# Optimization experiments

Measured on AMD Instinct MI355X. Metric: run time of the kernel, lower is better.

## Reference

```python
import jax, jax.numpy as jnp
import numpy as np

IN_FEATURES = 512
OUT_FEATURES = 10
NEURONS_STRUCTURES = [64, 128, 256, 512]
REPETITIONS = 5
NUM_ACTIVATIONS = 4  # relu, tanh, sigmoid, gelu (exact erf, matching torch nn.GELU)
NUM_MODELS = NUM_ACTIVATIONS * REPETITIONS * len(NEURONS_STRUCTURES)  # 80
TOTAL_HIDDEN = sum(NEURONS_STRUCTURES) * REPETITIONS * NUM_ACTIVATIONS  # 19200
BATCH = 1024


def _build_neuron_model_id():
    # Mirrors ParallelMLPs.__init__ construction order:
    # for act -> for rep -> for structure: assign consecutive model ids
    ids = []
    m = 0
    for _act in range(NUM_ACTIVATIONS):
        for _rep in range(REPETITIONS):
            for n in NEURONS_STRUCTURES:
                ids += [m] * n
                m += 1
    return np.asarray(ids, dtype=np.int32)


def setup_inputs() -> dict:
    key = jax.random.key(0)
    k1, k2, k3, k4, k5 = jax.random.split(key, 5)
    x = jax.random.normal(k1, (BATCH, IN_FEATURES), dtype=jnp.float32)
    hidden_w = jax.random.normal(k2, (TOTAL_HIDDEN, IN_FEATURES), dtype=jnp.float32) * 0.05
    hidden_b = jax.random.normal(k3, (TOTAL_HIDDEN,), dtype=jnp.float32) * 0.05
    out_w = jax.random.normal(k4, (OUT_FEATURES, TOTAL_HIDDEN), dtype=jnp.float32) * 0.05
    out_b = jax.random.normal(k5, (NUM_MODELS, OUT_FEATURES), dtype=jnp.float32) * 0.05
    neuron_model_id = jnp.asarray(_build_neuron_model_id())
    return {"x": x, "hidden_w": hidden_w, "hidden_b": hidden_b,
            "out_w": out_w, "out_b": out_b, "neuron_model_id": neuron_model_id}


def reference(x, hidden_w, hidden_b, out_w, out_b, neuron_model_id):
    # Shared hidden linear: [B, H]
    h = x @ hidden_w.T + hidden_b
    # Per-block activations on equal contiguous chunks of the hidden dim
    split = TOTAL_HIDDEN // NUM_ACTIVATIONS
    acts = [jax.nn.relu, jnp.tanh, jax.nn.sigmoid,
            lambda t: jax.nn.gelu(t, approximate=False)]
    a = jnp.concatenate(
        [f(h[:, i * split:(i + 1) * split]) for i, f in enumerate(acts)], axis=1)
    # Ragged grouped out-projection: contrib[h, b, o] = a[b, h] * out_w[o, h]
    contrib = a.T[:, :, None] * out_w.T[:, None, :]  # [H, B, O]
    grouped = jax.ops.segment_sum(contrib, neuron_model_id,
                                  num_segments=NUM_MODELS)  # [M, B, O]
    return jnp.transpose(grouped, (1, 0, 2)) + out_b[None, :, :]  # [B, M, O]
```

## Files before the change

### kernel.cpp

```cpp
#include <hip/hip_runtime.h>
#include <hip/hip_bf16.h>
#include <cstdint>
#include <cstddef>


typedef unsigned short u16;
typedef unsigned int u32;
typedef __bf16 bf16x8 __attribute__((ext_vector_type(8)));
typedef float f32x4 __attribute__((ext_vector_type(4)));

__device__ __forceinline__ u16 f2bf(float f) {
  u32 u = __builtin_bit_cast(u32, f);
  u += 0x7fffu + ((u >> 16) & 1u);
  return (u16)(u >> 16);
}

__device__ __forceinline__ void async16(void* l, const void* g) {
  __builtin_amdgcn_global_load_lds(
      (__attribute__((address_space(1))) void*)(void*)g,
      (__attribute__((address_space(3))) void*)l, 16, 0, 0);
}

__device__ __forceinline__ void drain_vm() {
  asm volatile("s_waitcnt vmcnt(0)" ::: "memory");
}

__global__ __launch_bounds__(256) void cvt_kernel(
    const float4* __restrict__ xs, uint2* __restrict__ xd, int nx4,
    const float4* __restrict__ ws, uint2* __restrict__ wd, int nw4) {
  int i = blockIdx.x * blockDim.x + threadIdx.x;
  if (i >= nx4 + nw4) return;
  const float4* s; uint2* d; int j;
  if (i < nx4) { s = xs; d = xd; j = i; }
  else         { s = ws; d = wd; j = i - nx4; }
  float4 f = s[j];
  uint2 o;
  o.x = (u32)f2bf(f.x) | ((u32)f2bf(f.y) << 16);
  o.y = (u32)f2bf(f.z) | ((u32)f2bf(f.w) << 16);
  d[j] = o;
}

__global__ __launch_bounds__(256, 2) void gemm_act_kernel(
    const u16* __restrict__ A,
    const u16* __restrict__ Bw,
    const float* __restrict__ hbias,
    u16* __restrict__ aout) {
  __shared__ char lds[65536];
  const int t = threadIdx.x;
  const int lane = t & 63;
  const int w = t >> 6;
  const int c = blockIdx.x & 7;
  const int L = c * 150 + (blockIdx.x >> 3);
  const int bx = L >> 3;
  const int by = L & 7;
  const int row0 = by * 128;
  const int col0 = bx * 128;
  const int wr = w >> 1, wc = w & 1;

  f32x4 acc[4][4];
#pragma unroll
  for (int m = 0; m < 4; ++m)
#pragma unroll
    for (int n = 0; n < 4; ++n)
#pragma unroll
      for (int r = 0; r < 4; ++r) acc[m][n][r] = 0.f;

  const int srow = t >> 3;
  const int sc8 = t & 7;

  auto stage = [&](int buf, int kt) {
    const int k0 = kt * 64 + sc8 * 8;
#pragma unroll
    for (int i = 0; i < 4; ++i) {
      int row = i * 32 + srow;
      async16(lds + buf * 16384 + i * 4096 + w * 1024,
              A + (size_t)(row0 + row) * 512 + k0);
      async16(lds + 32768 + buf * 16384 + i * 4096 + w * 1024,
              Bw + (size_t)(col0 + row) * 512 + k0);
    }
  };

  const int il = lane & 15, q = lane >> 4;

  auto compute = [&](int buf) {
    const char* bA = lds + buf * 16384;
    const char* bB = lds + 32768 + buf * 16384;
#pragma unroll
    for (int ks = 0; ks < 2; ++ks) {
      bf16x8 av[4], bv[4];
#pragma unroll
      for (int m = 0; m < 4; ++m)
        av[m] = *(const bf16x8*)(bA + (wr * 64 + m * 16 + il) * 128 + ks * 64 + q * 16);
#pragma unroll
      for (int n = 0; n < 4; ++n)
        bv[n] = *(const bf16x8*)(bB + (wc * 64 + n * 16 + il) * 128 + ks * 64 + q * 16);
#pragma unroll
      for (int m = 0; m < 4; ++m)
#pragma unroll
        for (int n = 0; n < 4; ++n)
          acc[m][n] = __builtin_amdgcn_mfma_f32_16x16x32_bf16(av[m], bv[n],
                                                              acc[m][n], 0, 0, 0);
    }
  };

  stage(0, 0);
  drain_vm();
  __syncthreads();
  for (int kt = 0; kt < 8; ++kt) {
    int cur = kt & 1;
    if (kt < 7) stage(cur ^ 1, kt + 1);
    compute(cur);
    drain_vm();
    __syncthreads();
  }

#pragma unroll
  for (int n = 0; n < 4; ++n) {
    int gcol = col0 + wc * 64 + n * 16 + il;
    int act = gcol / 4800;
    float bias = hbias[gcol];
#pragma unroll
    for (int m = 0; m < 4; ++m) {
      int growb = row0 + wr * 64 + m * 16 + q * 4;
#pragma unroll
      for (int r = 0; r < 4; ++r) {
        float v = acc[m][n][r] + bias;
        float o;
        if (act == 0)      o = fmaxf(v, 0.f);
        else if (act == 1) o = tanhf(v);
        else if (act == 2) o = 1.f / (1.f + __expf(-v));
        else               o = 0.5f * v * (1.f + erff(v * 0.70710678118f));
        aout[(size_t)(growb + r) * 19200 + gcol] = f2bf(o);
      }
    }
  }
}

__global__ __launch_bounds__(256) void layer2_kernel(
    const u16* __restrict__ a,
    const float* __restrict__ ow,
    const float* __restrict__ ob,
    float* __restrict__ out) {
  const int t = threadIdx.x;
  const int lane = t & 63;
  const int w = t >> 6;
  const int m = blockIdx.x % 80;
  const int bt = blockIdx.x / 80;
  const int b0 = bt * 64 + w * 16;
  const int s = m & 3;
  const int rep = (m >> 2) % 5;
  const int act = m / 20;
  const int seg0 = act * 4800 + rep * 960 + 64 * ((1 << s) - 1);
  const int K = 64 << s;
  const int il = lane & 15, q = lane >> 4;

  f32x4 acc = {0.f, 0.f, 0.f, 0.f};
  const u16* arow = a + (size_t)(b0 + il) * 19200 + seg0 + q * 8;
  const float* wrow = ow + il * 19200 + seg0 + q * 8;
  const bool wvalid = il < 10;

  for (int k0 = 0; k0 < K; k0 += 32) {
    bf16x8 af = *(const bf16x8*)(arow + k0);
    union { bf16x8 v; u16 u[8]; } bb;
    if (wvalid) {
      float4 f0 = *(const float4*)(wrow + k0);
      float4 f1 = *(const float4*)(wrow + k0 + 4);
      bb.u[0] = f2bf(f0.x); bb.u[1] = f2bf(f0.y);
      bb.u[2] = f2bf(f0.z); bb.u[3] = f2bf(f0.w);
      bb.u[4] = f2bf(f1.x); bb.u[5] = f2bf(f1.y);
      bb.u[6] = f2bf(f1.z); bb.u[7] = f2bf(f1.w);
    } else {
#pragma unroll
      for (int j = 0; j < 8; ++j) bb.u[j] = 0;
    }
    acc = __builtin_amdgcn_mfma_f32_16x16x32_bf16(af, bb.v, acc, 0, 0, 0);
  }

  if (il < 10) {
    float bias = ob[m * 10 + il];
#pragma unroll
    for (int r = 0; r < 4; ++r)
      out[(size_t)(b0 + q * 4 + r) * 800 + m * 10 + il] = acc[r] + bias;
  }
}

extern "C" void kernel_launch(void* const* d_in, const int* in_sizes, int n_in,
                              void* d_out, int out_size, void* d_ws, size_t ws_size,
                              hipStream_t stream) {
  const float* x = (const float*)d_in[0];
  const float* hw = (const float*)d_in[1];
  const float* hb = (const float*)d_in[2];
  const float* ow = (const float*)d_in[3];
  const float* ob = (const float*)d_in[4];
  float* out = (float*)d_out;

  char* ws = (char*)d_ws;
  u16* xb = (u16*)ws;
  u16* wb = (u16*)(ws + 1048576);
  u16* ab = (u16*)(ws + 1048576 + 19660800);

  const int nx4 = (1024 * 512) / 4;
  const int nw4 = (19200 * 512) / 4;
  const int tot = nx4 + nw4;
  cvt_kernel<<<tot / 256, 256, 0, stream>>>((const float4*)x, (uint2*)xb, nx4,
                                            (const float4*)hw, (uint2*)wb, nw4);
  gemm_act_kernel<<<1200, 256, 0, stream>>>(xb, wb, hb, ab);
  layer2_kernel<<<1280, 256, 0, stream>>>(ab, ow, ob, out);
}
```

Measured before the change: 182.6 us.

## Swizzle LDS tiles, prefetch two stages ahead, and use exp-based tanh

XOR-swizzles the 16-byte chunk index within each 128-byte LDS row, on both the async global-to-LDS writes and the MFMA fragment reads, to cut LDS bank conflicts. The K loop now keeps two tiles in flight: it waits with a partial vmcnt, uses raw s_barrier instead of draining all loads each iteration, and issues the load for tile kt+2 after compute. tanhf is replaced with a formula built on __expf, which trades some accuracy for a cheaper epilogue. The partial-wait counts must match the number of outstanding loads per thread, or tiles could be read before they arrive.

```diff
diff --git a/kernel.cpp b/kernel.cpp
--- a/kernel.cpp
+++ b/kernel.cpp
@@ -19,10 +19,6 @@
   __builtin_amdgcn_global_load_lds(
       (__attribute__((address_space(1))) void*)(void*)g,
       (__attribute__((address_space(3))) void*)l, 16, 0, 0);
-}
-
-__device__ __forceinline__ void drain_vm() {
-  asm volatile("s_waitcnt vmcnt(0)" ::: "memory");
 }
 
 __global__ __launch_bounds__(256) void cvt_kernel(
@@ -69,7 +65,8 @@
   const int sc8 = t & 7;
 
   auto stage = [&](int buf, int kt) {
-    const int k0 = kt * 64 + sc8 * 8;
+    const int c8 = sc8 ^ (srow & 7);
+    const int k0 = kt * 64 + c8 * 8;
 #pragma unroll
     for (int i = 0; i < 4; ++i) {
       int row = i * 32 + srow;
@@ -89,11 +86,17 @@
     for (int ks = 0; ks < 2; ++ks) {
       bf16x8 av[4], bv[4];
 #pragma unroll
-      for (int m = 0; m < 4; ++m)
-        av[m] = *(const bf16x8*)(bA + (wr * 64 + m * 16 + il) * 128 + ks * 64 + q * 16);
-#pragma unroll
-      for (int n = 0; n < 4; ++n)
-        bv[n] = *(const bf16x8*)(bB + (wc * 64 + n * 16 + il) * 128 + ks * 64 + q * 16);
+      for (int m = 0; m < 4; ++m) {
+        int row = wr * 64 + m * 16 + il;
+        av[m] = *(const bf16x8*)(bA + row * 128 +
+                                 ((ks * 64 + q * 16) ^ ((row & 7) << 4)));
+      }
+#pragma unroll
+      for (int n = 0; n < 4; ++n) {
+        int row = wc * 64 + n * 16 + il;
+        bv[n] = *(const bf16x8*)(bB + row * 128 +
+                                 ((ks * 64 + q * 16) ^ ((row & 7) << 4)));
+      }
 #pragma unroll
       for (int m = 0; m < 4; ++m)
 #pragma unroll
@@ -104,14 +107,16 @@
   };
 
   stage(0, 0);
-  drain_vm();
-  __syncthreads();
+  stage(1, 1);
+#pragma unroll
   for (int kt = 0; kt < 8; ++kt) {
-    int cur = kt & 1;
-    if (kt < 7) stage(cur ^ 1, kt + 1);
-    compute(cur);
-    drain_vm();
-    __syncthreads();
+    if (kt < 7) asm volatile("s_waitcnt vmcnt(8)" ::: "memory");
+    else        asm volatile("s_waitcnt vmcnt(0)" ::: "memory");
+    __builtin_amdgcn_s_barrier();
+    compute(kt & 1);
+    asm volatile("" ::: "memory");
+    __builtin_amdgcn_s_barrier();
+    if (kt < 6) stage(kt & 1, kt + 2);
   }
 
 #pragma unroll
@@ -127,7 +132,10 @@
         float v = acc[m][n][r] + bias;
         float o;
         if (act == 0)      o = fmaxf(v, 0.f);
-        else if (act == 1) o = tanhf(v);
+        else if (act == 1) {
+          float e = __expf(-2.f * fabsf(v));
+          o = copysignf((1.f - e) / (1.f + e), v);
+        }
         else if (act == 2) o = 1.f / (1.f + __expf(-v));
         else               o = 0.5f * v * (1.f + erff(v * 0.70710678118f));
         aout[(size_t)(growb + r) * 19200 + gcol] = f2bf(o);
```

Result: faster. 177.0 us (-3.0%).
